# Performance work log

Hardware: AMD Instinct MI355X
Metric: run time of the kernel (lower is better)

## Reference

```python
import jax, jax.numpy as jnp
import numpy as np

B, L, EMBED = 8, 4096, 1024
HEADS, WIN, SHIFT = 16, 128, 64
HD = EMBED // HEADS
MLP_HIDDEN = 4 * EMBED
SCALE = HD ** -0.5
NW = L // WIN


def _layer_norm(x, w, b, eps=1e-5):
    m = x.mean(-1, keepdims=True)
    v = x.var(-1, keepdims=True)
    return (x - m) * jax.lax.rsqrt(v + eps) * w + b


def _compute_mask():
    # replicate SwinBlock1D._compute_mask: region ids over full L, then windowed
    sizes = [L - WIN, WIN - SHIFT, SHIFT]
    region = np.zeros(L, np.int32)
    pos = 0
    for i, s in enumerate(sizes):
        region[pos:pos + s] = i
        pos += s
    region = region.reshape(NW, WIN)
    diff = region[:, None, :] - region[:, :, None]  # (nW, W, W)
    return jnp.asarray(np.where(diff != 0, -100.0, 0.0).astype(np.float32))


_MASK = _compute_mask()
_REL_IDX = jnp.arange(WIN)[None, :] - jnp.arange(WIN)[:, None] + WIN - 1  # (W, W)


def setup_inputs() -> dict:
    key = jax.random.key(0)
    ks = jax.random.split(key, 8)
    s = 0.02

    def w(k, shape):
        return jax.random.normal(k, shape, jnp.float32) * s

    return {
        "x": jax.random.normal(ks[0], (B, L, EMBED), jnp.float32),
        "qkv_w": w(ks[1], (3 * EMBED, EMBED)),
        "qkv_b": jnp.zeros((3 * EMBED,), jnp.float32),
        "proj_w": w(ks[2], (EMBED, EMBED)),
        "proj_b": jnp.zeros((EMBED,), jnp.float32),
        "rpb": w(ks[3], (2 * WIN - 1, HEADS)),
        "norm1_w": jnp.ones((EMBED,), jnp.float32),
        "norm1_b": jnp.zeros((EMBED,), jnp.float32),
        "norm2_w": jnp.ones((EMBED,), jnp.float32),
        "norm2_b": jnp.zeros((EMBED,), jnp.float32),
        "mlp_w1": w(ks[4], (MLP_HIDDEN, EMBED)),
        "mlp_b1": jnp.zeros((MLP_HIDDEN,), jnp.float32),
        "mlp_w2": w(ks[5], (EMBED, MLP_HIDDEN)),
        "mlp_b2": jnp.zeros((EMBED,), jnp.float32),
    }


def reference(x, qkv_w, qkv_b, proj_w, proj_b, rpb,
              norm1_w, norm1_b, norm2_w, norm2_b,
              mlp_w1, mlp_b1, mlp_w2, mlp_b2):
    BW = B * NW
    shortcut = x
    h = _layer_norm(x, norm1_w, norm1_b)
    # shifted-window attention (shift_size > 0)
    h = jnp.roll(h, -SHIFT, axis=1)
    win = h.reshape(BW, WIN, EMBED)
    qkv = (win @ qkv_w.T + qkv_b).reshape(BW, WIN, 3, HEADS, HD)
    qkv = qkv.transpose(2, 0, 3, 1, 4)  # (3, BW, H, W, hd)
    q, k, v = qkv[0], qkv[1], qkv[2]
    attn = jnp.einsum('bhqd,bhkd->bhqk', q, k) * SCALE
    bias = rpb[_REL_IDX]  # (W, W, H)
    attn = attn + bias.transpose(2, 0, 1)[None]
    attn = attn.reshape(B, NW, HEADS, WIN, WIN) + _MASK[None, :, None]
    attn = jax.nn.softmax(attn.reshape(BW, HEADS, WIN, WIN), axis=-1)
    # dropout layers are identity in eval mode
    out = jnp.einsum('bhqk,bhkd->bhqd', attn, v)
    out = out.transpose(0, 2, 1, 3).reshape(BW, WIN, EMBED)
    out = out @ proj_w.T + proj_b
    out = out.reshape(B, L, EMBED)
    out = jnp.roll(out, SHIFT, axis=1)
    x = shortcut + out
    # MLP block
    h2 = _layer_norm(x, norm2_w, norm2_b)
    h2 = jax.nn.gelu(h2 @ mlp_w1.T + mlp_b1, approximate=False) @ mlp_w2.T + mlp_b2
    return x + h2
```

## Files before the change

kernel.cpp:

```cpp
#include <hip/hip_runtime.h>
#include <cstdint>
#include <cstddef>

#define SEQ_L   4096
#define EMBED   1024
#define HEADS   16
#define WINSZ   128
#define SHIFTSZ 64
#define HD      64
#define NWIN    32
#define MTOT    32768
#define ATT_SCALE 0.125f

typedef __bf16 bf16x8 __attribute__((ext_vector_type(8)));
typedef float  f32x4  __attribute__((ext_vector_type(4)));

typedef __attribute__((address_space(3))) void       lds_void;
typedef const __attribute__((address_space(1))) void gbl_void;

#define GLDS16(g, s) __builtin_amdgcn_global_load_lds((gbl_void*)(g), (lds_void*)(s), 16, 0, 0)

__device__ __forceinline__ unsigned short f2bf(float f) {
    unsigned int u = __float_as_uint(f);
    u += 0x7fffu + ((u >> 16) & 1u);
    return (unsigned short)(u >> 16);
}

__launch_bounds__(256)
__global__ void wconv4(const float* __restrict__ s0, const float* __restrict__ s1,
                       const float* __restrict__ s2, const float* __restrict__ s3,
                       unsigned short* __restrict__ d0, unsigned short* __restrict__ d1,
                       unsigned short* __restrict__ d2, unsigned short* __restrict__ d3)
{
    const int b = blockIdx.x;
    const float* s; unsigned short* d; int off;
    if (b < 3072)      { s = s0; d = d0; off = b; }
    else if (b < 4096) { s = s1; d = d1; off = b - 3072; }
    else if (b < 8192) { s = s2; d = d2; off = b - 4096; }
    else               { s = s3; d = d3; off = b - 8192; }
    const int i = (off * 256 + threadIdx.x) * 4;
    const float4 v = *(const float4*)(s + i);
    ushort4 o;
    o.x = f2bf(v.x); o.y = f2bf(v.y); o.z = f2bf(v.z); o.w = f2bf(v.w);
    *(ushort4*)(d + i) = o;
}

__launch_bounds__(256)
__global__ void ln_kernel(const float* __restrict__ x, const float* __restrict__ gw,
                          const float* __restrict__ gb, unsigned short* __restrict__ out,
                          int shift)
{
    const int row  = blockIdx.x * 4 + (threadIdx.x >> 6);
    const int lane = threadIdx.x & 63;
    const int b    = row >> 12;
    const int lw   = row & 4095;
    const int src  = (b << 12) | ((lw + shift) & 4095);
    const float* xr = x + (size_t)src * EMBED;

    float4 v[4];
    float s = 0.f, q = 0.f;
#pragma unroll
    for (int j = 0; j < 4; ++j) {
        v[j] = ((const float4*)xr)[lane + j * 64];
        s += v[j].x + v[j].y + v[j].z + v[j].w;
        q += v[j].x * v[j].x + v[j].y * v[j].y + v[j].z * v[j].z + v[j].w * v[j].w;
    }
#pragma unroll
    for (int off = 32; off > 0; off >>= 1) {
        s += __shfl_xor(s, off);
        q += __shfl_xor(q, off);
    }
    const float mean = s * (1.0f / 1024.0f);
    const float rstd = rsqrtf(q * (1.0f / 1024.0f) - mean * mean + 1e-5f);

    unsigned short* orow = out + (size_t)row * EMBED;
#pragma unroll
    for (int j = 0; j < 4; ++j) {
        const float4 w4 = ((const float4*)gw)[lane + j * 64];
        const float4 b4 = ((const float4*)gb)[lane + j * 64];
        ushort4 o;
        o.x = f2bf((v[j].x - mean) * rstd * w4.x + b4.x);
        o.y = f2bf((v[j].y - mean) * rstd * w4.y + b4.y);
        o.z = f2bf((v[j].z - mean) * rstd * w4.z + b4.z);
        o.w = f2bf((v[j].w - mean) * rstd * w4.w + b4.w);
        ((ushort4*)orow)[lane + j * 64] = o;
    }
}


__device__ __forceinline__ void stage_half(const unsigned short* __restrict__ g, int ldk,
                                           char* ldsbase, int tid)
{
    const int r  = tid >> 3;
    const int cg = ((tid & 7) ^ (r & 7)) << 3;
    GLDS16(g + (size_t)r        * ldk + cg, ldsbase + tid * 16);
    GLDS16(g + (size_t)(r + 64) * ldk + cg, ldsbase + 8192 + tid * 16);
}

__device__ __forceinline__ bf16x8 lds_frag(const char* half, int row, int koff)
{
    const int off = koff ^ ((row & 7) << 4);
    return *(const bf16x8*)(half + row * 128 + off);
}

template<int EPI>
__launch_bounds__(512, 2)
__global__ void gemm256(const unsigned short* __restrict__ A, const unsigned short* __restrict__ W,
                        const float* __restrict__ bias, void* __restrict__ outv,
                        const float* __restrict__ resid, int M, int N, int K)
{
    __shared__ __align__(16) char lds[131072];
    const int tid = threadIdx.x;
    const int l   = tid & 63, w = tid >> 6;
    const int wm  = w >> 2, wn = w & 3;
    const int lr  = l & 15, hi = l >> 4;
    const int k0off = hi << 4;
    const int br0   = (wn & 1) << 6;

    int id = blockIdx.x;
    const int nwg = gridDim.x;
    id = (id & 7) * (nwg >> 3) + (id >> 3);
    const int Ntl = N >> 8;
    const int m0  = (id / Ntl) << 8;
    const int n0  = (id % Ntl) << 8;
    const int NT  = K >> 6;

#define HTB(b, ab, h) (lds + ((((b) << 1 | (ab)) << 1 | (h)) << 14))

    stage_half(A + (size_t)m0         * K, K, HTB(0,0,0), tid);
    stage_half(A + (size_t)(m0 + 128) * K, K, HTB(0,0,1), tid);
    stage_half(W + (size_t)n0         * K, K, HTB(0,1,0), tid);
    stage_half(W + (size_t)(n0 + 128) * K, K, HTB(0,1,1), tid);
    asm volatile("s_waitcnt vmcnt(0)" ::: "memory");
    __builtin_amdgcn_s_barrier();

    f32x4 acc[8][4];
#pragma unroll
    for (int f = 0; f < 8; ++f)
#pragma unroll
        for (int n = 0; n < 4; ++n)
            acc[f][n] = (f32x4){0.f, 0.f, 0.f, 0.f};

    bf16x8 bf[4][2], af0[2][2], af1[2][2];

#define LOAD_A_BANK(bank, AHP, F0)                                          \
    af##bank[0][0] = lds_frag(AHP, (F0) * 16 + lr,      k0off);             \
    af##bank[0][1] = lds_frag(AHP, (F0) * 16 + lr,      64 + k0off);        \
    af##bank[1][0] = lds_frag(AHP, (F0) * 16 + 16 + lr, k0off);             \
    af##bank[1][1] = lds_frag(AHP, (F0) * 16 + 16 + lr, 64 + k0off);

#define MFMA_BANK(bank, F0)                                                 \
    __builtin_amdgcn_s_setprio(1);                                          \
    _Pragma("unroll")                                                       \
    for (int n = 0; n < 4; ++n) {                                           \
        acc[F0][n]       = __builtin_amdgcn_mfma_f32_16x16x32_bf16(af##bank[0][0], bf[n][0], acc[F0][n], 0, 0, 0);       \
        acc[F0][n]       = __builtin_amdgcn_mfma_f32_16x16x32_bf16(af##bank[0][1], bf[n][1], acc[F0][n], 0, 0, 0);       \
        acc[(F0) + 1][n] = __builtin_amdgcn_mfma_f32_16x16x32_bf16(af##bank[1][0], bf[n][0], acc[(F0) + 1][n], 0, 0, 0); \
        acc[(F0) + 1][n] = __builtin_amdgcn_mfma_f32_16x16x32_bf16(af##bank[1][1], bf[n][1], acc[(F0) + 1][n], 0, 0, 0); \
    }                                                                       \
    __builtin_amdgcn_s_setprio(0);

#define TILE(BUF)                                                              \
    {                                                                          \
        const char* Ah = HTB(BUF, 0, wm);                                      \
        const char* Bh = HTB(BUF, 1, wn >> 1);                                 \
                                                        \
        _Pragma("unroll")                                                      \
        for (int n = 0; n < 4; ++n) {                                          \
            bf[n][0] = lds_frag(Bh, br0 + n * 16 + lr, k0off);                 \
            bf[n][1] = lds_frag(Bh, br0 + n * 16 + lr, 64 + k0off);            \
        }                                                                      \
        LOAD_A_BANK(0, Ah, 0)                                                  \
                                           \
        if (t + 1 < NT) {                                                      \
            const unsigned short* An = A + (size_t)m0 * K + (size_t)(t + 1) * 64; \
            const unsigned short* Wn = W + (size_t)n0 * K + (size_t)(t + 1) * 64; \
            stage_half(An,                   K, HTB(BUF ^ 1, 0, 0), tid);      \
            stage_half(An + (size_t)128 * K, K, HTB(BUF ^ 1, 0, 1), tid);      \
            stage_half(Wn,                   K, HTB(BUF ^ 1, 1, 0), tid);      \
            stage_half(Wn + (size_t)128 * K, K, HTB(BUF ^ 1, 1, 1), tid);      \
        }                                                                      \
        LOAD_A_BANK(1, Ah, 2)                                                  \
        asm volatile("s_waitcnt lgkmcnt(4)" ::: "memory");                     \
        MFMA_BANK(0, 0)                                                        \
        LOAD_A_BANK(0, Ah, 4)                                                  \
        asm volatile("s_waitcnt lgkmcnt(4)" ::: "memory");                     \
        MFMA_BANK(1, 2)                                                        \
        LOAD_A_BANK(1, Ah, 6)                                                  \
        asm volatile("s_waitcnt lgkmcnt(4)" ::: "memory");                     \
        MFMA_BANK(0, 4)                                                        \
        asm volatile("s_waitcnt lgkmcnt(0)" ::: "memory");                     \
        MFMA_BANK(1, 6)                                                        \
        asm volatile("s_waitcnt vmcnt(0)" ::: "memory");                       \
        __builtin_amdgcn_s_barrier();                                          \
    }

    int t;
    for (int u = 0; u < (NT >> 1); ++u) {
        t = 2 * u;     TILE(0)
        t = 2 * u + 1; TILE(1)
    }
#undef TILE
#undef LOAD_A_BANK
#undef MFMA_BANK
#undef HTB

    const int cb = n0 + wn * 64;
    float bv[4];
#pragma unroll
    for (int n = 0; n < 4; ++n) bv[n] = bias[cb + n * 16 + lr];

#pragma unroll
    for (int f = 0; f < 8; ++f) {
        const int mbase = m0 + wm * 128 + f * 16 + hi * 4;
#pragma unroll
        for (int n = 0; n < 4; ++n) {
            const int col = cb + n * 16 + lr;
#pragma unroll
            for (int r = 0; r < 4; ++r) {
                const int m = mbase + r;
                float v = acc[f][n][r] + bv[n];
                if constexpr (EPI == 0) {
                    ((unsigned short*)outv)[(size_t)m * N + col] = f2bf(v);
                } else if constexpr (EPI == 1) {
                    const int bb = m >> 12;
                    const int lw = m & 4095;
                    const int ll = (lw + SHIFTSZ) & 4095;
                    const size_t di = ((size_t)(bb << 12) + ll) * (size_t)N + col;
                    ((float*)outv)[di] = resid[di] + v;
                } else if constexpr (EPI == 2) {
                    const float g = 0.5f * v * (1.0f + erff(v * 0.70710678118654752f));
                    ((unsigned short*)outv)[(size_t)m * N + col] = f2bf(g);
                } else {
                    float* o = (float*)outv;
                    const size_t di = (size_t)m * N + col;
                    o[di] = o[di] + v;
                }
            }
        }
    }
}

#define SM_VT  34816
#define SM_RPB 52224

__device__ __forceinline__ bf16x8 vt_frag(const char* vt, int d, int kbyte)
{
    const int key = ((d >> 3) & 7) << 4;
    return *(const bf16x8*)(vt + d * 272 + (kbyte ^ key));
}

__launch_bounds__(256, 3)
__global__ void attn_kernel(const unsigned short* __restrict__ qkv, const float* __restrict__ rpb,
                            unsigned short* __restrict__ outp)
{
    __shared__ __align__(16) char smem[53248];

    const int t   = threadIdx.x;
    const int l   = t & 63;
    const int w   = t >> 6;
    const int lr  = l & 15;
    const int lq  = l >> 4;
    const int lk  = lq * 8;
    const int blk = blockIdx.x;
    const int win = blk >> 4;
    const int h   = blk & 15;
    const bool masked = ((win & (NWIN - 1)) == NWIN - 1);

    const unsigned short* qb = qkv + (size_t)(win * WINSZ) * (3 * EMBED) + h * HD;
    const unsigned short* kb = qb + EMBED;
    const unsigned short* vb = qb + 2 * EMBED;
    const int mrow = w * 32;
    float* rpbl = (float*)(smem + SM_RPB);

    bf16x8 aqr[2][2];
#pragma unroll
    for (int ks = 0; ks < 2; ++ks)
#pragma unroll
        for (int mi = 0; mi < 2; ++mi)
            aqr[ks][mi] = *(const bf16x8*)(qb + (size_t)(mrow + mi * 16 + lr) * (3 * EMBED) + ks * 32 + lk);

    if (t < 255) rpbl[t] = rpb[t * HEADS + h];

    {
        const int c = t & 7;
#pragma unroll
        for (int p = 0; p < 4; ++p) {
            const int r  = (t >> 3) + p * 32;
            const int cg = (c ^ (r & 7)) << 3;
            GLDS16(kb + (size_t)r * (3 * EMBED) + cg, smem + p * 4096 + t * 16);
        }
    }
    {
        const int c = t & 7;
#pragma unroll
        for (int p = 0; p < 4; ++p) {
            const int k = (t >> 3) + p * 32;
            const uint4 v = *(const uint4*)(vb + (size_t)k * (3 * EMBED) + c * 8);
            const unsigned int vals[4] = {v.x, v.y, v.z, v.w};
            char* base = smem + SM_VT;
#pragma unroll
            for (int e2 = 0; e2 < 4; ++e2) {
                const int d0 = c * 8 + e2 * 2;
                const int key = c << 4;
                *(unsigned short*)(base + d0 * 272 + ((2 * k) ^ key))       = (unsigned short)(vals[e2] & 0xffff);
                *(unsigned short*)(base + (d0 + 1) * 272 + ((2 * k) ^ key)) = (unsigned short)(vals[e2] >> 16);
            }
        }
    }
    asm volatile("s_waitcnt vmcnt(0)" ::: "memory");
    __syncthreads();

    f32x4 sacc[2][8];
#pragma unroll
    for (int a = 0; a < 2; ++a)
#pragma unroll
        for (int b = 0; b < 8; ++b)
            sacc[a][b] = (f32x4){0.f, 0.f, 0.f, 0.f};

#pragma unroll
    for (int ks = 0; ks < 2; ++ks) {
        const int kby = ks * 64 + lq * 16;
        bf16x8 bk8[8];
#pragma unroll
        for (int ni = 0; ni < 8; ++ni)
            bk8[ni] = lds_frag(smem, ni * 16 + lr, kby);
#pragma unroll
        for (int mi = 0; mi < 2; ++mi)
#pragma unroll
            for (int ni = 0; ni < 8; ++ni)
                sacc[mi][ni] = __builtin_amdgcn_mfma_f32_16x16x32_bf16(aqr[ks][mi], bk8[ni], sacc[mi][ni], 0, 0, 0);
    }

    __syncthreads();

#pragma unroll
    for (int mi = 0; mi < 2; ++mi)
#pragma unroll
        for (int r = 0; r < 4; ++r) {
            const int i = mrow + mi * 16 + lq * 4 + r;
            float v[8];
            float mx = -1e30f;
#pragma unroll
            for (int ni = 0; ni < 8; ++ni) {
                const int j = ni * 16 + lr;
                float sv = sacc[mi][ni][r] * ATT_SCALE + rpbl[j - i + WINSZ - 1];
                if (masked && ((i >= SHIFTSZ) != (j >= SHIFTSZ))) sv -= 100.0f;
                v[ni] = sv;
                mx = fmaxf(mx, sv);
            }
#pragma unroll
            for (int s = 1; s < 16; s <<= 1) mx = fmaxf(mx, __shfl_xor(mx, s));
            float sm = 0.f;
#pragma unroll
            for (int ni = 0; ni < 8; ++ni) {
                const float p = __expf(v[ni] - mx);
                v[ni] = p;
                sm += p;
            }
#pragma unroll
            for (int s = 1; s < 16; s <<= 1) sm += __shfl_xor(sm, s);
            const float rs = 1.0f / sm;
#pragma unroll
            for (int ni = 0; ni < 8; ++ni)
                *(unsigned short*)(smem + ((size_t)i * 136 + ni * 16 + lr) * 2) = f2bf(v[ni] * rs);
        }

    __syncthreads();

    f32x4 oacc[2][4];
#pragma unroll
    for (int a = 0; a < 2; ++a)
#pragma unroll
        for (int b = 0; b < 4; ++b)
            oacc[a][b] = (f32x4){0.f, 0.f, 0.f, 0.f};

#pragma unroll
    for (int ks = 0; ks < 4; ++ks) {
        const int k0 = ks * 32;
        bf16x8 ap[2], av[4];
#pragma unroll
        for (int mi = 0; mi < 2; ++mi)
            ap[mi] = *(const bf16x8*)(smem + ((size_t)(mrow + mi * 16 + lr) * 136 + k0 + lk) * 2);
#pragma unroll
        for (int ni = 0; ni < 4; ++ni)
            av[ni] = vt_frag(smem + SM_VT, ni * 16 + lr, k0 * 2 + lq * 16);
#pragma unroll
        for (int mi = 0; mi < 2; ++mi)
#pragma unroll
            for (int ni = 0; ni < 4; ++ni)
                oacc[mi][ni] = __builtin_amdgcn_mfma_f32_16x16x32_bf16(ap[mi], av[ni], oacc[mi][ni], 0, 0, 0);
    }

    unsigned short* ob = outp + (size_t)(win * WINSZ) * EMBED + h * HD;
#pragma unroll
    for (int mi = 0; mi < 2; ++mi)
#pragma unroll
        for (int ni = 0; ni < 4; ++ni)
#pragma unroll
            for (int r = 0; r < 4; ++r) {
                const int i = mrow + mi * 16 + lq * 4 + r;
                const int d = ni * 16 + lr;
                ob[(size_t)i * EMBED + d] = f2bf(oacc[mi][ni][r]);
            }
}

extern "C" void kernel_launch(void* const* d_in, const int* in_sizes, int n_in,
                              void* d_out, int out_size, void* d_ws, size_t ws_size,
                              hipStream_t stream)
{
    const float* x      = (const float*)d_in[0];
    const float* qkv_w  = (const float*)d_in[1];
    const float* qkv_b  = (const float*)d_in[2];
    const float* proj_w = (const float*)d_in[3];
    const float* proj_b = (const float*)d_in[4];
    const float* rpb    = (const float*)d_in[5];
    const float* n1w    = (const float*)d_in[6];
    const float* n1b    = (const float*)d_in[7];
    const float* n2w    = (const float*)d_in[8];
    const float* n2b    = (const float*)d_in[9];
    const float* w1     = (const float*)d_in[10];
    const float* b1     = (const float*)d_in[11];
    const float* w2     = (const float*)d_in[12];
    const float* b2     = (const float*)d_in[13];
    float* out = (float*)d_out;

    unsigned short* wqkv  = (unsigned short*)d_ws;
    unsigned short* wproj = wqkv  + (size_t)3072 * 1024;
    unsigned short* wm1   = wproj + (size_t)1024 * 1024;
    unsigned short* wm2   = wm1   + (size_t)4096 * 1024;
    unsigned short* bufA  = wm2   + (size_t)4096 * 1024;
    unsigned short* bufB  = bufA  + (size_t)MTOT * EMBED;

    wconv4<<<12288, 256, 0, stream>>>(qkv_w, proj_w, w1, w2, wqkv, wproj, wm1, wm2);

    ln_kernel<<<8192, 256, 0, stream>>>(x, n1w, n1b, bufA, SHIFTSZ);

    gemm256<0><<<dim3(1536), 512, 0, stream>>>(bufA, wqkv, qkv_b, bufB, nullptr, MTOT, 3 * EMBED, EMBED);

    attn_kernel<<<4096, 256, 0, stream>>>(bufB, rpb, bufA);

    gemm256<1><<<dim3(512), 512, 0, stream>>>(bufA, wproj, proj_b, out, x, MTOT, EMBED, EMBED);

    ln_kernel<<<8192, 256, 0, stream>>>(out, n2w, n2b, bufA, 0);

    for (int c = 0; c < 2; ++c) {
        const size_t r0 = (size_t)c * 16384;
        gemm256<2><<<dim3(1024), 512, 0, stream>>>(bufA + r0 * EMBED, wm1, b1, bufB, nullptr,
                                                   16384, 4 * EMBED, EMBED);
        gemm256<3><<<dim3(256), 512, 0, stream>>>(bufB, wm2, b2, out + r0 * EMBED, nullptr,
                                                  16384, EMBED, 4 * EMBED);
    }
}
```

Before: 1.137 ms.

## Halve attention P buffer in LDS to raise occupancy, defer softmax normalization

The attention kernel now writes the probability matrix to LDS in two 64-column halves with an XOR swizzle, reusing a 16KB buffer instead of a padded 34KB one. That cuts shared memory from 53KB to 34KB so launch bounds can allow 4 blocks per CU instead of 3. Softmax normalization moves to the output epilogue by scaling with the saved row-sum reciprocal, and the row max is kept so the second half's exponentials can be recomputed. The cost is an extra pair of barriers, the second half's exp being recomputed, and more live registers (sacc, max, reciprocals) that may cause spills at the tighter launch bound.

```diff
diff --git a/kernel.cpp b/kernel.cpp
--- a/kernel.cpp
+++ b/kernel.cpp
@@ -87,7 +87,6 @@
     }
 }
 
-
 __device__ __forceinline__ void stage_half(const unsigned short* __restrict__ g, int ldk,
                                            char* ldsbase, int tid)
 {
@@ -164,14 +163,12 @@
     {                                                                          \
         const char* Ah = HTB(BUF, 0, wm);                                      \
         const char* Bh = HTB(BUF, 1, wn >> 1);                                 \
-                                                        \
         _Pragma("unroll")                                                      \
         for (int n = 0; n < 4; ++n) {                                          \
             bf[n][0] = lds_frag(Bh, br0 + n * 16 + lr, k0off);                 \
             bf[n][1] = lds_frag(Bh, br0 + n * 16 + lr, 64 + k0off);            \
         }                                                                      \
         LOAD_A_BANK(0, Ah, 0)                                                  \
-                                           \
         if (t + 1 < NT) {                                                      \
             const unsigned short* An = A + (size_t)m0 * K + (size_t)(t + 1) * 64; \
             const unsigned short* Wn = W + (size_t)n0 * K + (size_t)(t + 1) * 64; \
@@ -241,8 +238,8 @@
     }
 }
 
-#define SM_VT  34816
-#define SM_RPB 52224
+#define SM_VT  16384
+#define SM_RPB 33792
 
 __device__ __forceinline__ bf16x8 vt_frag(const char* vt, int d, int kbyte)
 {
@@ -250,11 +247,11 @@
     return *(const bf16x8*)(vt + d * 272 + (kbyte ^ key));
 }
 
-__launch_bounds__(256, 3)
+__launch_bounds__(256, 4)
 __global__ void attn_kernel(const unsigned short* __restrict__ qkv, const float* __restrict__ rpb,
                             unsigned short* __restrict__ outp)
 {
-    __shared__ __align__(16) char smem[53248];
+    __shared__ __align__(16) char smem[34816];
 
     const int t   = threadIdx.x;
     const int l   = t & 63;
@@ -334,6 +331,7 @@
 
     __syncthreads();
 
+    float rsv[2][4], mxv[2][4];
 #pragma unroll
     for (int mi = 0; mi < 2; ++mi)
 #pragma unroll
@@ -360,10 +358,12 @@
             }
 #pragma unroll
             for (int s = 1; s < 16; s <<= 1) sm += __shfl_xor(sm, s);
-            const float rs = 1.0f / sm;
-#pragma unroll
-            for (int ni = 0; ni < 8; ++ni)
-                *(unsigned short*)(smem + ((size_t)i * 136 + ni * 16 + lr) * 2) = f2bf(v[ni] * rs);
+            rsv[mi][r] = 1.0f / sm;
+            mxv[mi][r] = mx;
+            const int key = (i & 7) << 4;
+#pragma unroll
+            for (int ni = 0; ni < 4; ++ni)
+                *(unsigned short*)(smem + i * 128 + ((ni * 32 + lr * 2) ^ key)) = f2bf(v[ni]);
         }
 
     __syncthreads();
@@ -376,15 +376,54 @@
             oacc[a][b] = (f32x4){0.f, 0.f, 0.f, 0.f};
 
 #pragma unroll
-    for (int ks = 0; ks < 4; ++ks) {
-        const int k0 = ks * 32;
+    for (int ksh = 0; ksh < 2; ++ksh) {
         bf16x8 ap[2], av[4];
 #pragma unroll
+        for (int mi = 0; mi < 2; ++mi) {
+            const int ri = mrow + mi * 16 + lr;
+            ap[mi] = *(const bf16x8*)(smem + ri * 128 + ((ksh * 64 + lq * 16) ^ ((ri & 7) << 4)));
+        }
+#pragma unroll
+        for (int ni = 0; ni < 4; ++ni)
+            av[ni] = vt_frag(smem + SM_VT, ni * 16 + lr, ksh * 64 + lq * 16);
+#pragma unroll
         for (int mi = 0; mi < 2; ++mi)
-            ap[mi] = *(const bf16x8*)(smem + ((size_t)(mrow + mi * 16 + lr) * 136 + k0 + lk) * 2);
+#pragma unroll
+            for (int ni = 0; ni < 4; ++ni)
+                oacc[mi][ni] = __builtin_amdgcn_mfma_f32_16x16x32_bf16(ap[mi], av[ni], oacc[mi][ni], 0, 0, 0);
+    }
+
+    __syncthreads();
+
+#pragma unroll
+    for (int mi = 0; mi < 2; ++mi)
+#pragma unroll
+        for (int r = 0; r < 4; ++r) {
+            const int i = mrow + mi * 16 + lq * 4 + r;
+            const float mx = mxv[mi][r];
+            const int key = (i & 7) << 4;
+#pragma unroll
+            for (int ni = 4; ni < 8; ++ni) {
+                const int j = ni * 16 + lr;
+                float sv = sacc[mi][ni][r] * ATT_SCALE + rpbl[j - i + WINSZ - 1];
+                if (masked && ((i >= SHIFTSZ) != (j >= SHIFTSZ))) sv -= 100.0f;
+                *(unsigned short*)(smem + i * 128 + (((ni - 4) * 32 + lr * 2) ^ key)) = f2bf(__expf(sv - mx));
+            }
+        }
+
+    __syncthreads();
+
+#pragma unroll
+    for (int ksh = 0; ksh < 2; ++ksh) {
+        bf16x8 ap[2], av[4];
+#pragma unroll
+        for (int mi = 0; mi < 2; ++mi) {
+            const int ri = mrow + mi * 16 + lr;
+            ap[mi] = *(const bf16x8*)(smem + ri * 128 + ((ksh * 64 + lq * 16) ^ ((ri & 7) << 4)));
+        }
 #pragma unroll
         for (int ni = 0; ni < 4; ++ni)
-            av[ni] = vt_frag(smem + SM_VT, ni * 16 + lr, k0 * 2 + lq * 16);
+            av[ni] = vt_frag(smem + SM_VT, ni * 16 + lr, 128 + ksh * 64 + lq * 16);
 #pragma unroll
         for (int mi = 0; mi < 2; ++mi)
 #pragma unroll
@@ -401,7 +440,7 @@
             for (int r = 0; r < 4; ++r) {
                 const int i = mrow + mi * 16 + lq * 4 + r;
                 const int d = ni * 16 + lr;
-                ob[(size_t)i * EMBED + d] = f2bf(oacc[mi][ni][r]);
+                ob[(size_t)i * EMBED + d] = f2bf(oacc[mi][ni][r] * rsv[mi][r]);
             }
 }
 
```

Result: slower. 1.244 ms (+9.4%).
